# Kernel optimization log

Measured on AMD Instinct MI355X. Metric: run time of the kernel, lower is better.

Reference implementation:

```python
import jax, jax.numpy as jnp
import numpy as np

N, L, FEAT = 16, 4096, 512
DIN = 21 * 14 * 3 + FEAT  # 1394
EPS = 1e-6


def setup_inputs() -> dict:
    key = jax.random.key(0)
    ks = jax.random.split(key, 12)

    def lin_w(k, i, o):
        return (jax.random.normal(k, (i, o), jnp.float32) / np.sqrt(i)).astype(jnp.float32)

    return {
        "aa": jax.random.randint(ks[0], (N, L), 0, 21),
        "pos14": jax.random.normal(ks[1], (N, L, 14, 3), jnp.float32),
        "atom_mask": jax.random.bernoulli(ks[2], 0.9, (N, L, 14)),
        "embed": (jax.random.normal(ks[3], (21, FEAT), jnp.float32) * 0.02),
        "w1": lin_w(ks[4], DIN, 2 * FEAT),
        "b1": jnp.zeros((2 * FEAT,), jnp.float32),
        "w2": lin_w(ks[5], 2 * FEAT, FEAT),
        "b2": jnp.zeros((FEAT,), jnp.float32),
        "w3": lin_w(ks[6], FEAT, FEAT),
        "b3": jnp.zeros((FEAT,), jnp.float32),
        "w4": lin_w(ks[7], FEAT, FEAT),
        "b4": jnp.zeros((FEAT,), jnp.float32),
    }


def _normalize(v):
    return v / (jnp.linalg.norm(v, axis=-1, keepdims=True) + EPS)


def reference(aa, pos14, atom_mask, embed, w1, b1, w2, b2, w3, b3, w4, b4):
    n, l = aa.shape
    # --- frame construction: center=CA (atom 1), p1=C (atom 2), p2=N (atom 0)
    center = pos14[:, :, 1]
    v1 = pos14[:, :, 2] - center
    e1 = _normalize(v1)
    v2 = pos14[:, :, 0] - center
    u2 = v2 - jnp.sum(e1 * v2, axis=-1, keepdims=True) * e1  # Gram-Schmidt
    e2 = _normalize(u2)
    e3 = jnp.cross(e1, e2)
    R = jnp.stack([e1, e2, e3], axis=-1)  # (N,L,3,3), columns [e1,e2,e3]

    # --- global_to_local: p = R^T (q - t)
    q = pos14 - center[:, :, None, :]            # (N,L,14,3)
    crd14 = jnp.einsum('nlij,nlai->nlaj', R, q)  # (N,L,14,3)
    crd14 = jnp.where(atom_mask[..., None], crd14, 0.0)

    # --- one-hot residue placement (equivalent to the (N,L,21,14,3) expand+where)
    onehot = jax.nn.one_hot(aa, 21, dtype=crd14.dtype)             # (N,L,21)
    crd_feat = (onehot[..., None] * crd14.reshape(n, l, 1, 14 * 3))
    crd_feat = crd_feat.reshape(n, l, 21 * 14 * 3)                  # (N,L,882)

    aa_feat = embed[aa]                                             # (N,L,FEAT)
    h = jnp.concatenate([crd_feat, aa_feat], axis=-1)               # (N,L,1394)
    h = jax.nn.relu(h @ w1 + b1)
    h = jax.nn.relu(h @ w2 + b2)
    h = jax.nn.relu(h @ w3 + b3)
    return h @ w4 + b4
```

## Files before the change

### kernel.cpp

```cpp
#include <hip/hip_runtime.h>
#include <hip/hip_bf16.h>


typedef __attribute__((ext_vector_type(8))) short short8;
typedef __attribute__((ext_vector_type(4))) float floatx4;

#define TOKENS 65536
#define FEATD 512
#define L1OUT 1024
#define NAA 21
#define EPSF 1e-6f
#define ORDER_N 66880

static __device__ __forceinline__ unsigned short f2bf(float f) {
  union { float f; unsigned int u; } v; v.f = f;
  unsigned int u = v.u;
  return (unsigned short)((u + 0x7FFFu + ((u >> 16) & 1u)) >> 16);
}

#define GLDS16(g, l) __builtin_amdgcn_global_load_lds(                        \
    (const __attribute__((address_space(1))) unsigned int*)(g),               \
    (__attribute__((address_space(3))) unsigned int*)(l), 16, 0, 0)

__global__ void k_init(int* __restrict__ order, int* __restrict__ counts,
                       const unsigned int* __restrict__ mask) {
  int i = blockIdx.x * 256 + threadIdx.x;
  if (i < ORDER_N) order[i] = -1;
  if (blockIdx.x == 0) {
    if (threadIdx.x < 64) counts[threadIdx.x] = 0;
    __syncthreads();
    unsigned int v = mask[threadIdx.x];
    int b = 0;
    if (v == 0x3F800000u) b = 2;
    else if (v > 1u) b = 1;
    if (b) atomicOr(&counts[32], b);
  }
}

__global__ void k_prep(const float* __restrict__ w2, unsigned short* __restrict__ w2T,
                       const float* __restrict__ w3, unsigned short* __restrict__ w3T,
                       const float* __restrict__ w4, unsigned short* __restrict__ w4T,
                       const float* __restrict__ w1, unsigned short* __restrict__ w1T2,
                       const float* __restrict__ embed, const float* __restrict__ b1,
                       float* __restrict__ T1) {
  const int b = blockIdx.x;
  const int tid = threadIdx.x;
  if (b < 4096) {
    const float* W; unsigned short* WT; int kbits, N, idx;
    if (b < 2048)      { W = w2; WT = w2T; kbits = 10; N = 512; idx = b * 256 + tid; }
    else if (b < 3072) { W = w3; WT = w3T; kbits = 9;  N = 512; idx = (b - 2048) * 256 + tid; }
    else               { W = w4; WT = w4T; kbits = 9;  N = 512; idx = (b - 3072) * 256 + tid; }
    int K = 1 << kbits;
    int n = idx >> kbits, k = idx & (K - 1);
    WT[(size_t)n * K + k] = f2bf(W[(size_t)k * N + n]);
  } else if (b < 4180) {
    int idx = (b - 4096) * 256 + tid;
    int a = idx >> 10, c = idx & 1023;
    unsigned short tmp[64];
#pragma unroll
    for (int k = 0; k < 64; ++k)
      tmp[k] = (k < 42) ? f2bf(w1[(size_t)(a * 42 + k) * L1OUT + c]) : 0;
    uint4* dst = (uint4*)&w1T2[(size_t)idx * 64];
#pragma unroll
    for (int q = 0; q < 8; ++q) dst[q] = ((const uint4*)tmp)[q];
  } else {
    int idx = (b - 4180) * 256 + tid;
    int a = idx >> 10, c = idx & 1023;
    float acc = b1[c];
    const float* e = embed + a * FEATD;
#pragma unroll 8
    for (int k = 0; k < FEATD; ++k)
      acc += e[k] * w1[(size_t)(882 + k) * L1OUT + c];
    T1[idx] = acc;
  }
}

__global__ void k_feat(const float* __restrict__ pos14, const int* __restrict__ aa,
                       const void* __restrict__ maskp, unsigned short* __restrict__ crdb,
                       int* __restrict__ counts) {
  __shared__ int hist[NAA];
  const int tid = threadIdx.x;
  if (tid < NAA) hist[tid] = 0;
  __syncthreads();
  const int t = blockIdx.x * 256 + tid;
  const int fl = counts[32];
  const float* p = pos14 + (size_t)t * 42;
  float px[14], py[14], pz[14];
#pragma unroll
  for (int a = 0; a < 14; ++a) { px[a] = p[a*3]; py[a] = p[a*3+1]; pz[a] = p[a*3+2]; }
  float cx = px[1], cy = py[1], cz = pz[1];
  float v1x = px[2]-cx, v1y = py[2]-cy, v1z = pz[2]-cz;
  float n1 = sqrtf(v1x*v1x + v1y*v1y + v1z*v1z);
  float i1 = 1.f / (n1 + EPSF);
  float e1x = v1x*i1, e1y = v1y*i1, e1z = v1z*i1;
  float v2x = px[0]-cx, v2y = py[0]-cy, v2z = pz[0]-cz;
  float d12 = e1x*v2x + e1y*v2y + e1z*v2z;
  float u2x = v2x - d12*e1x, u2y = v2y - d12*e1y, u2z = v2z - d12*e1z;
  float n2 = sqrtf(u2x*u2x + u2y*u2y + u2z*u2z);
  float i2 = 1.f / (n2 + EPSF);
  float e2x = u2x*i2, e2y = u2y*i2, e2z = u2z*i2;
  float e3x = e1y*e2z - e1z*e2y;
  float e3y = e1z*e2x - e1x*e2z;
  float e3z = e1x*e2y - e1y*e2x;
  unsigned short ob[64];
#pragma unroll
  for (int a = 0; a < 14; ++a) {
    bool mv;
    size_t mi = (size_t)t * 14 + a;
    if (fl & 2)      mv = ((const float*)maskp)[mi] != 0.f;
    else if (fl & 1) mv = ((const unsigned char*)maskp)[mi] != 0;
    else             mv = ((const int*)maskp)[mi] != 0;
    float qx = px[a]-cx, qy = py[a]-cy, qz = pz[a]-cz;
    ob[a*3+0] = mv ? f2bf(e1x*qx + e1y*qy + e1z*qz) : 0;
    ob[a*3+1] = mv ? f2bf(e2x*qx + e2y*qy + e2z*qz) : 0;
    ob[a*3+2] = mv ? f2bf(e3x*qx + e3y*qy + e3z*qz) : 0;
  }
#pragma unroll
  for (int k = 42; k < 64; ++k) ob[k] = 0;
  uint4* dst = (uint4*)&crdb[(size_t)t * 64];
#pragma unroll
  for (int q = 0; q < 8; ++q) dst[q] = ((const uint4*)ob)[q];
  atomicAdd(&hist[aa[t]], 1);
  __syncthreads();
  if (tid < NAA && hist[tid]) atomicAdd(&counts[tid], hist[tid]);
}

__global__ void k_offsets(const int* __restrict__ counts, int* __restrict__ cnt2) {
  if (threadIdx.x == 0) {
    int run = 0;
    for (int a = 0; a < NAA; ++a) { cnt2[a] = run; run += ((counts[a] + 63) >> 6) << 6; }
  }
}

__global__ void k_scatter(const int* __restrict__ aa, int* __restrict__ cnt2,
                          int* __restrict__ order) {
  __shared__ int lh[NAA], base[NAA];
  const int tid = threadIdx.x;
  if (tid < NAA) lh[tid] = 0;
  __syncthreads();
  const int t = blockIdx.x * 256 + tid;
  const int a = aa[t];
  const int r = atomicAdd(&lh[a], 1);
  __syncthreads();
  if (tid < NAA) base[tid] = lh[tid] ? atomicAdd(&cnt2[tid], lh[tid]) : 0;
  __syncthreads();
  order[base[a] + r] = t;
}

__global__ void k_layer1(const int* __restrict__ order, const int* __restrict__ aa_g,
                         const unsigned short* __restrict__ crdb,
                         const unsigned short* __restrict__ w1T2,
                         const float* __restrict__ T1, unsigned short* __restrict__ h1) {
  __shared__ int tokens[64];
  __shared__ int s_aa;
  __shared__ unsigned short Al[64 * 64];
  __shared__ unsigned short Bl[256 * 64];
  const int tid = threadIdx.x;
  const int lane = tid & 63;
  const int wid = tid >> 6;
  const int pb = blockIdx.y;
  const int cc = blockIdx.x * 256;
  if (tid < 64) tokens[tid] = order[pb * 64 + tid];
  __syncthreads();
  if (tid == 0) {
    int a = -1;
    for (int i = 0; i < 64; ++i) if (tokens[i] >= 0) { a = aa_g[tokens[i]]; break; }
    s_aa = a;
  }
  __syncthreads();
  const int a = s_aa;
  if (a < 0) return;
  const int lrow = lane >> 3;
  const int gch = (lane & 7) ^ lrow;
#pragma unroll
  for (int i = 0; i < 2; ++i) {
    int row = wid * 16 + i * 8;
    int tok = tokens[row + lrow]; if (tok < 0) tok = 0;
    GLDS16(&crdb[(size_t)tok * 64 + gch * 8], &Al[row * 64]);
  }
  const unsigned short* bsrc = w1T2 + ((size_t)a * L1OUT + cc) * 64;
#pragma unroll
  for (int i = 0; i < 8; ++i) {
    int row = wid * 64 + i * 8;
    GLDS16(&bsrc[(size_t)(row + lrow) * 64 + gch * 8], &Bl[row * 64]);
  }
  __syncthreads();
  const int wn = wid * 64;
  floatx4 acc[4][4] = {};
#pragma unroll
  for (int kk = 0; kk < 2; ++kk) {
    short8 af[4], bfr[4];
    const int kc = kk * 4 + (lane >> 4);
#pragma unroll
    for (int i = 0; i < 4; ++i) {
      int ar = i * 16 + (lane & 15);
      af[i]  = *(const short8*)&Al[ar * 64 + (kc ^ (ar & 7)) * 8];
      int br = wn + i * 16 + (lane & 15);
      bfr[i] = *(const short8*)&Bl[br * 64 + (kc ^ (br & 7)) * 8];
    }
#pragma unroll
    for (int i = 0; i < 4; ++i)
#pragma unroll
      for (int j = 0; j < 4; ++j)
        acc[i][j] = __builtin_amdgcn_mfma_f32_16x16x32_bf16(af[i], bfr[j], acc[i][j], 0, 0, 0);
  }
#pragma unroll
  for (int i = 0; i < 4; ++i) {
    int tb = i * 16 + ((lane >> 4) << 2);
#pragma unroll
    for (int j = 0; j < 4; ++j) {
      int colg = cc + wn + j * 16 + (lane & 15);
      float bv = T1[a * L1OUT + colg];
#pragma unroll
      for (int r = 0; r < 4; ++r) {
        int tok = tokens[tb + r];
        if (tok < 0) continue;
        h1[(size_t)tok * L1OUT + colg] = f2bf(fmaxf(acc[i][j][r] + bv, 0.f));
      }
    }
  }
}

template<int K, bool RELU, bool OUTBF16>
__global__ void k_gemm(const unsigned short* __restrict__ A,
                       const unsigned short* __restrict__ BT,
                       const float* __restrict__ bias, void* __restrict__ outp) {
  constexpr int N = 512;
  __shared__ unsigned short Al[128 * 64];
  __shared__ unsigned short Bl[128 * 64];
  const int l = blockIdx.x;
  const int m0 = (((l >> 5) << 3) | (l & 7)) * 128;
  const int n0 = ((l >> 3) & 3) * 128;
  const int tid = threadIdx.x;
  const int lane = tid & 63;
  const int wid = tid >> 6;
  const int wm = (wid & 1) * 64;
  const int wn = (wid >> 1) * 64;
  const int srow = wid * 32;
  const int lrow = lane >> 3;
  const int gcol = ((lane & 7) ^ lrow) * 8;
  floatx4 acc[4][4] = {};
  for (int k0 = 0; k0 < K; k0 += 64) {
#pragma unroll
    for (int i = 0; i < 4; ++i) {
      const int row = srow + i * 8;
      GLDS16(&A [(size_t)(m0 + row + lrow) * K + k0 + gcol], &Al[row * 64]);
      GLDS16(&BT[(size_t)(n0 + row + lrow) * K + k0 + gcol], &Bl[row * 64]);
    }
    __syncthreads();
#pragma unroll
    for (int kk = 0; kk < 2; ++kk) {
      short8 af[4], bfr[4];
      const int kc = kk * 4 + (lane >> 4);
      const int swz = (kc ^ (lane & 7)) * 8;
#pragma unroll
      for (int i = 0; i < 4; ++i) {
        af[i]  = *(const short8*)&Al[(wm + i * 16 + (lane & 15)) * 64 + swz];
        bfr[i] = *(const short8*)&Bl[(wn + i * 16 + (lane & 15)) * 64 + swz];
      }
#pragma unroll
      for (int i = 0; i < 4; ++i)
#pragma unroll
        for (int j = 0; j < 4; ++j)
          acc[i][j] = __builtin_amdgcn_mfma_f32_16x16x32_bf16(af[i], bfr[j], acc[i][j], 0, 0, 0);
    }
    __syncthreads();
  }
#pragma unroll
  for (int i = 0; i < 4; ++i) {
    int rbase = m0 + wm + i * 16 + ((lane >> 4) << 2);
#pragma unroll
    for (int j = 0; j < 4; ++j) {
      int col = n0 + wn + j * 16 + (lane & 15);
      float bv = bias[col];
#pragma unroll
      for (int r = 0; r < 4; ++r) {
        float v = acc[i][j][r] + bv;
        if (RELU) v = fmaxf(v, 0.f);
        size_t off = (size_t)(rbase + r) * N + col;
        if (OUTBF16) ((unsigned short*)outp)[off] = f2bf(v);
        else ((float*)outp)[off] = v;
      }
    }
  }
}

extern "C" void kernel_launch(void* const* d_in, const int* in_sizes, int n_in,
                              void* d_out, int out_size, void* d_ws, size_t ws_size,
                              hipStream_t stream) {
  const int*   aa    = (const int*)d_in[0];
  const float* pos14 = (const float*)d_in[1];
  const void*  mask  = d_in[2];
  const float* embed = (const float*)d_in[3];
  const float* w1    = (const float*)d_in[4];
  const float* b1    = (const float*)d_in[5];
  const float* w2    = (const float*)d_in[6];
  const float* b2    = (const float*)d_in[7];
  const float* w3    = (const float*)d_in[8];
  const float* b3    = (const float*)d_in[9];
  const float* w4    = (const float*)d_in[10];
  const float* b4    = (const float*)d_in[11];

  char* ws = (char*)d_ws;
  size_t o = 0;
  auto alloc = [&](size_t b) { size_t r = o; o += (b + 255) & ~(size_t)255; return r; };
  unsigned short* w2T = (unsigned short*)(ws + alloc((size_t)512 * 1024 * 2));
  unsigned short* w3T = (unsigned short*)(ws + alloc((size_t)512 * 512 * 2));
  unsigned short* w4T = (unsigned short*)(ws + alloc((size_t)512 * 512 * 2));
  unsigned short* w1T2 = (unsigned short*)(ws + alloc((size_t)NAA * 1024 * 64 * 2));
  float* T1   = (float*)(ws + alloc((size_t)NAA * 1024 * 4));
  unsigned short* crdb = (unsigned short*)(ws + alloc((size_t)TOKENS * 64 * 2));
  int* counts = (int*)(ws + alloc(64 * 4));
  int* cnt2   = (int*)(ws + alloc(64 * 4));
  int* order  = (int*)(ws + alloc((size_t)ORDER_N * 4));
  unsigned short* h1 = (unsigned short*)(ws + alloc((size_t)TOKENS * 1024 * 2));
  unsigned short* h2 = (unsigned short*)(ws + alloc((size_t)TOKENS * 512 * 2));
  unsigned short* h3 = h1;

  k_init<<<262, 256, 0, stream>>>(order, counts, (const unsigned int*)mask);
  k_prep<<<4264, 256, 0, stream>>>(w2, w2T, w3, w3T, w4, w4T, w1, w1T2, embed, b1, T1);
  k_feat<<<256, 256, 0, stream>>>(pos14, aa, mask, crdb, counts);
  k_offsets<<<1, 64, 0, stream>>>(counts, cnt2);
  k_scatter<<<256, 256, 0, stream>>>(aa, cnt2, order);
  k_layer1<<<dim3(4, 1045), 256, 0, stream>>>(order, aa, crdb, w1T2, T1, h1);
  k_gemm<1024, true,  true ><<<2048, 256, 0, stream>>>(h1, w2T, b2, h2);
  k_gemm<512,  true,  true ><<<2048, 256, 0, stream>>>(h2, w3T, b3, h3);
  k_gemm<512,  false, false><<<2048, 256, 0, stream>>>(h3, w4T, b4, d_out);
}
```

Measured before the change: 437.6 us.

## Rewrite dense GEMMs as 256x256 double-buffered, interleaved-prefetch MFMA kernel

Replaces the 128x128 single-buffered GEMM used for layers 2-4 with a 256x256 tile kernel of 512 threads. It uses two LDS buffers, prefetches tile t+2 during compute through staged global_load_lds calls, and waits on vmcnt instead of a full sync. The MFMA blocks are interleaved with fragment loads and raised in priority. This aims to hide global-load latency and raise data reuse per tile, at the cost of far more LDS (128KB per block) and registers, which lowers occupancy.

```diff
diff --git a/kernel.cpp b/kernel.cpp
--- a/kernel.cpp
+++ b/kernel.cpp
@@ -222,57 +222,119 @@
 }
 
 template<int K, bool RELU, bool OUTBF16>
-__global__ void k_gemm(const unsigned short* __restrict__ A,
-                       const unsigned short* __restrict__ BT,
-                       const float* __restrict__ bias, void* __restrict__ outp) {
+__global__ __launch_bounds__(512, 2)
+void k_gemm256(const unsigned short* __restrict__ A,
+               const unsigned short* __restrict__ BT,
+               const float* __restrict__ bias, void* __restrict__ outp) {
   constexpr int N = 512;
-  __shared__ unsigned short Al[128 * 64];
-  __shared__ unsigned short Bl[128 * 64];
+  constexpr int NKT = K / 64;
+  __shared__ unsigned short Al[2][256 * 64];
+  __shared__ unsigned short Bl[2][256 * 64];
   const int l = blockIdx.x;
-  const int m0 = (((l >> 5) << 3) | (l & 7)) * 128;
-  const int n0 = ((l >> 3) & 3) * 128;
+  const int x = l & 7;
+  const int c = l >> 3;
+  const int m0 = (x * 32 + (c >> 1)) * 256;
+  const int n0 = (c & 1) * 256;
   const int tid = threadIdx.x;
   const int lane = tid & 63;
   const int wid = tid >> 6;
-  const int wm = (wid & 1) * 64;
-  const int wn = (wid >> 1) * 64;
-  const int srow = wid * 32;
+  const int wm2 = (wid & 1) * 128;
+  const int wn2 = (wid >> 1) * 64;
   const int lrow = lane >> 3;
   const int gcol = ((lane & 7) ^ lrow) * 8;
-  floatx4 acc[4][4] = {};
-  for (int k0 = 0; k0 < K; k0 += 64) {
-#pragma unroll
-    for (int i = 0; i < 4; ++i) {
-      const int row = srow + i * 8;
-      GLDS16(&A [(size_t)(m0 + row + lrow) * K + k0 + gcol], &Al[row * 64]);
-      GLDS16(&BT[(size_t)(n0 + row + lrow) * K + k0 + gcol], &Bl[row * 64]);
-    }
-    __syncthreads();
-#pragma unroll
-    for (int kk = 0; kk < 2; ++kk) {
-      short8 af[4], bfr[4];
-      const int kc = kk * 4 + (lane >> 4);
-      const int swz = (kc ^ (lane & 7)) * 8;
-#pragma unroll
-      for (int i = 0; i < 4; ++i) {
-        af[i]  = *(const short8*)&Al[(wm + i * 16 + (lane & 15)) * 64 + swz];
-        bfr[i] = *(const short8*)&Bl[(wn + i * 16 + (lane & 15)) * 64 + swz];
-      }
-#pragma unroll
-      for (int i = 0; i < 4; ++i)
-#pragma unroll
-        for (int j = 0; j < 4; ++j)
-          acc[i][j] = __builtin_amdgcn_mfma_f32_16x16x32_bf16(af[i], bfr[j], acc[i][j], 0, 0, 0);
-    }
-    __syncthreads();
-  }
-#pragma unroll
-  for (int i = 0; i < 4; ++i) {
-    int rbase = m0 + wm + i * 16 + ((lane >> 4) << 2);
+  const int ln = lane & 15;
+  const int sw0 = (((lane >> 4)    ) ^ (lane & 7)) * 8;
+  const int sw1 = ((4 + (lane >> 4)) ^ (lane & 7)) * 8;
+
+  const unsigned short* Ab = A  + (size_t)m0 * K;
+  const unsigned short* Bb = BT + (size_t)n0 * K;
+
+#define STAGE_A(kt, b, i)                                                     \
+  { const int row_ = (i) * 64 + wid * 8;                                      \
+    GLDS16(&Ab[(size_t)(row_ + lrow) * K + (kt) * 64 + gcol],                 \
+           &Al[b][row_ * 64]); }
+#define STAGE_B(kt, b, i)                                                     \
+  { const int row_ = (i) * 64 + wid * 8;                                      \
+    GLDS16(&Bb[(size_t)(row_ + lrow) * K + (kt) * 64 + gcol],                 \
+           &Bl[b][row_ * 64]); }
+
+  floatx4 acc[8][4] = {};
+
+#pragma unroll
+  for (int i = 0; i < 4; ++i) STAGE_A(0, 0, i);
+#pragma unroll
+  for (int i = 0; i < 4; ++i) STAGE_B(0, 0, i);
+#pragma unroll
+  for (int i = 0; i < 4; ++i) STAGE_A(1, 1, i);
+#pragma unroll
+  for (int i = 0; i < 4; ++i) STAGE_B(1, 1, i);
+
+  for (int t = 0; t < NKT; ++t) {
+    const int cur = t & 1;
+    if (t + 1 < NKT) { asm volatile("s_waitcnt vmcnt(8)" ::: "memory"); }
+    else             { asm volatile("s_waitcnt vmcnt(0)" ::: "memory"); }
+    __builtin_amdgcn_s_barrier();
+    __builtin_amdgcn_sched_barrier(0);
+    const unsigned short* Ac = &Al[cur][0];
+    const unsigned short* Bc = &Bl[cur][0];
+    const bool pf = (t + 2 < NKT);
+    short8 af[4][2], bq[2][2];
+
+#define LDA(frbase)                                                           \
+    _Pragma("unroll")                                                         \
+    for (int f = 0; f < 4; ++f) {                                             \
+      const int ro = (wm2 + ((frbase) + f) * 16 + ln) * 64;                   \
+      af[f][0] = *(const short8*)&Ac[ro + sw0];                               \
+      af[f][1] = *(const short8*)&Ac[ro + sw1];                               \
+    }
+#define LDB(fcbase)                                                           \
+    _Pragma("unroll")                                                         \
+    for (int cj = 0; cj < 2; ++cj) {                                          \
+      const int ro = (wn2 + ((fcbase) + cj) * 16 + ln) * 64;                  \
+      bq[cj][0] = *(const short8*)&Bc[ro + sw0];                              \
+      bq[cj][1] = *(const short8*)&Bc[ro + sw1];                              \
+    }
+#define MM(frbase, fcbase)                                                    \
+    __builtin_amdgcn_s_barrier();                                             \
+    __builtin_amdgcn_s_setprio(1);                                            \
+    _Pragma("unroll")                                                         \
+    for (int f = 0; f < 4; ++f)                                               \
+      _Pragma("unroll")                                                       \
+      for (int cj = 0; cj < 2; ++cj) {                                        \
+        acc[(frbase) + f][(fcbase) + cj] =                                    \
+          __builtin_amdgcn_mfma_f32_16x16x32_bf16(                            \
+            af[f][0], bq[cj][0], acc[(frbase) + f][(fcbase) + cj], 0, 0, 0);  \
+        acc[(frbase) + f][(fcbase) + cj] =                                    \
+          __builtin_amdgcn_mfma_f32_16x16x32_bf16(                            \
+            af[f][1], bq[cj][1], acc[(frbase) + f][(fcbase) + cj], 0, 0, 0);  \
+      }                                                                       \
+    __builtin_amdgcn_s_setprio(0);                                            \
+    __builtin_amdgcn_s_barrier();
+
+    LDA(0); LDB(0); MM(0, 0);
+    if (pf) { STAGE_A(t + 2, cur, 0); STAGE_A(t + 2, cur, 2); }
+    LDB(2); MM(0, 2);
+    LDA(4); MM(4, 2);
+    if (pf) { STAGE_A(t + 2, cur, 1); STAGE_A(t + 2, cur, 3); }
+    LDB(0); MM(4, 0);
+    if (pf) {
+      STAGE_B(t + 2, cur, 0); STAGE_B(t + 2, cur, 1);
+      STAGE_B(t + 2, cur, 2); STAGE_B(t + 2, cur, 3);
+    }
+#undef LDA
+#undef LDB
+#undef MM
+  }
+#undef STAGE_A
+#undef STAGE_B
+
+#pragma unroll
+  for (int i = 0; i < 8; ++i) {
+    const int rbase = m0 + wm2 + i * 16 + ((lane >> 4) << 2);
 #pragma unroll
     for (int j = 0; j < 4; ++j) {
-      int col = n0 + wn + j * 16 + (lane & 15);
-      float bv = bias[col];
+      const int col = n0 + wn2 + j * 16 + ln;
+      const float bv = bias[col];
 #pragma unroll
       for (int r = 0; r < 4; ++r) {
         float v = acc[i][j][r] + bv;
@@ -323,7 +385,7 @@
   k_offsets<<<1, 64, 0, stream>>>(counts, cnt2);
   k_scatter<<<256, 256, 0, stream>>>(aa, cnt2, order);
   k_layer1<<<dim3(4, 1045), 256, 0, stream>>>(order, aa, crdb, w1T2, T1, h1);
-  k_gemm<1024, true,  true ><<<2048, 256, 0, stream>>>(h1, w2T, b2, h2);
-  k_gemm<512,  true,  true ><<<2048, 256, 0, stream>>>(h2, w3T, b3, h3);
-  k_gemm<512,  false, false><<<2048, 256, 0, stream>>>(h3, w4T, b4, d_out);
-}
+  k_gemm256<1024, true,  true ><<<512, 512, 0, stream>>>(h1, w2T, b2, h2);
+  k_gemm256<512,  true,  true ><<<512, 512, 0, stream>>>(h2, w3T, b3, h3);
+  k_gemm256<512,  false, false><<<512, 512, 0, stream>>>(h3, w4T, b4, d_out);
+}
```

New measurement: 435.5 us. Within noise of the previous version (-0.5%).

## Use 256x256-tile double-buffered MFMA GEMM for layers two and three

Applied to the files above, without the earlier changes.

Adds a new GEMM kernel with 256x256 output tiles, 512 threads, double-buffered LDS staged through global_load_lds, XOR-swizzled LDS reads, and an interleaved prefetch/MFMA schedule with priority hints. Layers two and three switch to it, while the last fp32-output layer keeps the old kernel. Larger tiles raise operand reuse per byte loaded, and the explicit schedule tries to hide load latency behind MFMA work. In exchange, LDS use is large (128KB per block), occupancy drops to one block per CU, and only 512 blocks are launched.

```diff
diff --git a/kernel.cpp b/kernel.cpp
--- a/kernel.cpp
+++ b/kernel.cpp
@@ -285,6 +285,147 @@
   }
 }
 
+template<int K, bool RELU, bool OUTBF16>
+__global__ __launch_bounds__(512)
+void k_gemm256(const unsigned short* __restrict__ A,
+               const unsigned short* __restrict__ BT,
+               const float* __restrict__ bias, void* __restrict__ outp) {
+  constexpr int N = 512;
+  constexpr int NKT = K / 64;
+  constexpr int NITER = NKT / 2;
+  __shared__ unsigned short Al[2][256 * 64];
+  __shared__ unsigned short Bl[2][256 * 64];
+  const int l = blockIdx.x;
+  const int x = l & 7;
+  const int c = l >> 3;
+  const int m0 = (x * 32 + (c >> 1)) * 256;
+  const int n0 = (c & 1) * 256;
+  const int tid = threadIdx.x;
+  const int lane = tid & 63;
+  const int wid = tid >> 6;
+  const int wm2 = (wid & 1) * 128;
+  const int wn2 = (wid >> 1) * 64;
+  const int lrow = lane >> 3;
+  const int gcol = ((lane & 7) ^ lrow) * 8;
+  const int ln = lane & 15;
+  const int sw0 = (((lane >> 4)    ) ^ (lane & 7)) * 8;
+  const int sw1 = ((4 + (lane >> 4)) ^ (lane & 7)) * 8;
+
+  const unsigned short* Ab = A  + (size_t)m0 * K;
+  const unsigned short* Bb = BT + (size_t)n0 * K;
+
+#define STAGE_A(B, kt, i)                                                     \
+  { const int row_ = (i) * 64 + wid * 8;                                      \
+    GLDS16(&Ab[(size_t)(row_ + lrow) * K + (size_t)(kt) * 64 + gcol],         \
+           &Al[B][row_ * 64]); }
+#define STAGE_B(B, kt, i)                                                     \
+  { const int row_ = (i) * 64 + wid * 8;                                      \
+    GLDS16(&Bb[(size_t)(row_ + lrow) * K + (size_t)(kt) * 64 + gcol],         \
+           &Bl[B][row_ * 64]); }
+#define LDA(B, frbase, dst)                                                   \
+  _Pragma("unroll")                                                           \
+  for (int f = 0; f < 4; ++f) {                                               \
+    const int ro = (wm2 + ((frbase) + f) * 16 + ln) * 64;                     \
+    dst[f][0] = *(const short8*)&Al[B][ro + sw0];                             \
+    dst[f][1] = *(const short8*)&Al[B][ro + sw1];                             \
+  }
+#define LDB(B, fcbase, dst)                                                   \
+  _Pragma("unroll")                                                           \
+  for (int cj = 0; cj < 2; ++cj) {                                            \
+    const int ro = (wn2 + ((fcbase) + cj) * 16 + ln) * 64;                    \
+    dst[cj][0] = *(const short8*)&Bl[B][ro + sw0];                            \
+    dst[cj][1] = *(const short8*)&Bl[B][ro + sw1];                            \
+  }
+#define MMQ(frbase, fcbase, af, bq)                                           \
+  __builtin_amdgcn_s_setprio(1);                                              \
+  _Pragma("unroll")                                                           \
+  for (int kk = 0; kk < 2; ++kk)                                              \
+    _Pragma("unroll")                                                         \
+    for (int f = 0; f < 4; ++f)                                               \
+      _Pragma("unroll")                                                       \
+      for (int cj = 0; cj < 2; ++cj)                                          \
+        acc[(frbase) + f][(fcbase) + cj] =                                    \
+          __builtin_amdgcn_mfma_f32_16x16x32_bf16(                            \
+            af[f][kk], bq[cj][kk], acc[(frbase) + f][(fcbase) + cj], 0, 0, 0);\
+  __builtin_amdgcn_s_setprio(0);
+
+#define TILE4(B, kt2, dopf, WNend)                                            \
+  LDA(B, 0, afA); LDB(B, 0, bqA);                                             \
+  __builtin_amdgcn_sched_barrier(0);                                          \
+  __builtin_amdgcn_s_barrier();                                               \
+  MMQ(0, 0, afA, bqA);                                                        \
+  __builtin_amdgcn_s_barrier();                                               \
+  __builtin_amdgcn_sched_barrier(0);                                          \
+  if (dopf) { STAGE_A(B, kt2, 0); STAGE_A(B, kt2, 2); }                       \
+  LDA(B, 4, afB);                                                             \
+  __builtin_amdgcn_sched_barrier(0);                                          \
+  __builtin_amdgcn_s_barrier();                                               \
+  MMQ(4, 0, afB, bqA);                                                        \
+  __builtin_amdgcn_s_barrier();                                               \
+  __builtin_amdgcn_sched_barrier(0);                                          \
+  if (dopf) { STAGE_A(B, kt2, 1); STAGE_A(B, kt2, 3); }                       \
+  LDB(B, 2, bqB);                                                             \
+  __builtin_amdgcn_sched_barrier(0);                                          \
+  __builtin_amdgcn_s_barrier();                                               \
+  MMQ(4, 2, afB, bqB);                                                        \
+  __builtin_amdgcn_s_barrier();                                               \
+  __builtin_amdgcn_sched_barrier(0);                                          \
+  if (dopf) { STAGE_B(B, kt2, 0); STAGE_B(B, kt2, 1);                         \
+              STAGE_B(B, kt2, 2); STAGE_B(B, kt2, 3); }                       \
+  MMQ(0, 2, afA, bqB);                                                        \
+  asm volatile("s_waitcnt vmcnt(" #WNend ")" ::: "memory");                   \
+  __builtin_amdgcn_s_barrier();
+
+  floatx4 acc[8][4] = {};
+  short8 afA[4][2], afB[4][2], bqA[2][2], bqB[2][2];
+
+#pragma unroll
+  for (int i = 0; i < 4; ++i) STAGE_A(0, 0, i);
+#pragma unroll
+  for (int i = 0; i < 4; ++i) STAGE_B(0, 0, i);
+#pragma unroll
+  for (int i = 0; i < 4; ++i) STAGE_A(1, 1, i);
+#pragma unroll
+  for (int i = 0; i < 4; ++i) STAGE_B(1, 1, i);
+  asm volatile("s_waitcnt vmcnt(8)" ::: "memory");
+  __builtin_amdgcn_s_barrier();
+
+  for (int it = 0; it < NITER; ++it) {
+    const int te = 2 * it;
+    if (it + 1 < NITER) {
+      TILE4(0, te + 2, true, 8)
+      TILE4(1, te + 3, true, 8)
+    } else {
+      TILE4(0, te + 2, false, 0)
+      TILE4(1, te + 3, false, 0)
+    }
+  }
+#undef TILE4
+#undef MMQ
+#undef LDA
+#undef LDB
+#undef STAGE_A
+#undef STAGE_B
+
+#pragma unroll
+  for (int i = 0; i < 8; ++i) {
+    const int rbase = m0 + wm2 + i * 16 + ((lane >> 4) << 2);
+#pragma unroll
+    for (int j = 0; j < 4; ++j) {
+      const int col = n0 + wn2 + j * 16 + ln;
+      const float bv = bias[col];
+#pragma unroll
+      for (int r = 0; r < 4; ++r) {
+        float v = acc[i][j][r] + bv;
+        if (RELU) v = fmaxf(v, 0.f);
+        size_t off = (size_t)(rbase + r) * N + col;
+        if (OUTBF16) ((unsigned short*)outp)[off] = f2bf(v);
+        else ((float*)outp)[off] = v;
+      }
+    }
+  }
+}
+
 extern "C" void kernel_launch(void* const* d_in, const int* in_sizes, int n_in,
                               void* d_out, int out_size, void* d_ws, size_t ws_size,
                               hipStream_t stream) {
@@ -323,7 +464,7 @@
   k_offsets<<<1, 64, 0, stream>>>(counts, cnt2);
   k_scatter<<<256, 256, 0, stream>>>(aa, cnt2, order);
   k_layer1<<<dim3(4, 1045), 256, 0, stream>>>(order, aa, crdb, w1T2, T1, h1);
-  k_gemm<1024, true,  true ><<<2048, 256, 0, stream>>>(h1, w2T, b2, h2);
-  k_gemm<512,  true,  true ><<<2048, 256, 0, stream>>>(h2, w3T, b3, h3);
-  k_gemm<512,  false, false><<<2048, 256, 0, stream>>>(h3, w4T, b4, d_out);
-}
+  k_gemm256<1024, true,  true ><<<512, 512, 0, stream>>>(h1, w2T, b2, h2);
+  k_gemm256<512,  true,  true ><<<512, 512, 0, stream>>>(h2, w3T, b3, h3);
+  k_gemm<512, false, false><<<2048, 256, 0, stream>>>(h3, w4T, b4, d_out);
+}
```

Result: slower. 990.2 us (+126.2%).

## Fuse per-residue layer-1 GEMM into layer-2 GEMM, eliminating h1 buffer

Applied to the files above, without the earlier changes.

Replaces the separate layer-1 kernel and the first dense GEMM with one kernel that computes each 64-column chunk of h1 in shared memory from coordinate features and per-residue-type weights, then feeds it straight into the layer-2 MFMA accumulation. This removes writing and re-reading the large bf16 h1 intermediate from global memory. In exchange, layer-1 work is recomputed by each of the four output-column blocks, and a software-pipelined loop adds synchronization and LDS pressure. The order buffer is padded to match the 128-token tiling.

```diff
diff --git a/kernel.cpp b/kernel.cpp
--- a/kernel.cpp
+++ b/kernel.cpp
@@ -10,7 +10,7 @@
 #define L1OUT 1024
 #define NAA 21
 #define EPSF 1e-6f
-#define ORDER_N 66880
+#define ORDER_N 67072
 
 static __device__ __forceinline__ unsigned short f2bf(float f) {
   union { float f; unsigned int u; } v; v.f = f;
@@ -25,7 +25,7 @@
 __global__ void k_init(int* __restrict__ order, int* __restrict__ counts,
                        const unsigned int* __restrict__ mask) {
   int i = blockIdx.x * 256 + threadIdx.x;
-  if (i < ORDER_N) order[i] = -1;
+  order[i] = -1;
   if (blockIdx.x == 0) {
     if (threadIdx.x < 64) counts[threadIdx.x] = 0;
     __syncthreads();
@@ -147,80 +147,6 @@
   order[base[a] + r] = t;
 }
 
-__global__ void k_layer1(const int* __restrict__ order, const int* __restrict__ aa_g,
-                         const unsigned short* __restrict__ crdb,
-                         const unsigned short* __restrict__ w1T2,
-                         const float* __restrict__ T1, unsigned short* __restrict__ h1) {
-  __shared__ int tokens[64];
-  __shared__ int s_aa;
-  __shared__ unsigned short Al[64 * 64];
-  __shared__ unsigned short Bl[256 * 64];
-  const int tid = threadIdx.x;
-  const int lane = tid & 63;
-  const int wid = tid >> 6;
-  const int pb = blockIdx.y;
-  const int cc = blockIdx.x * 256;
-  if (tid < 64) tokens[tid] = order[pb * 64 + tid];
-  __syncthreads();
-  if (tid == 0) {
-    int a = -1;
-    for (int i = 0; i < 64; ++i) if (tokens[i] >= 0) { a = aa_g[tokens[i]]; break; }
-    s_aa = a;
-  }
-  __syncthreads();
-  const int a = s_aa;
-  if (a < 0) return;
-  const int lrow = lane >> 3;
-  const int gch = (lane & 7) ^ lrow;
-#pragma unroll
-  for (int i = 0; i < 2; ++i) {
-    int row = wid * 16 + i * 8;
-    int tok = tokens[row + lrow]; if (tok < 0) tok = 0;
-    GLDS16(&crdb[(size_t)tok * 64 + gch * 8], &Al[row * 64]);
-  }
-  const unsigned short* bsrc = w1T2 + ((size_t)a * L1OUT + cc) * 64;
-#pragma unroll
-  for (int i = 0; i < 8; ++i) {
-    int row = wid * 64 + i * 8;
-    GLDS16(&bsrc[(size_t)(row + lrow) * 64 + gch * 8], &Bl[row * 64]);
-  }
-  __syncthreads();
-  const int wn = wid * 64;
-  floatx4 acc[4][4] = {};
-#pragma unroll
-  for (int kk = 0; kk < 2; ++kk) {
-    short8 af[4], bfr[4];
-    const int kc = kk * 4 + (lane >> 4);
-#pragma unroll
-    for (int i = 0; i < 4; ++i) {
-      int ar = i * 16 + (lane & 15);
-      af[i]  = *(const short8*)&Al[ar * 64 + (kc ^ (ar & 7)) * 8];
-      int br = wn + i * 16 + (lane & 15);
-      bfr[i] = *(const short8*)&Bl[br * 64 + (kc ^ (br & 7)) * 8];
-    }
-#pragma unroll
-    for (int i = 0; i < 4; ++i)
-#pragma unroll
-      for (int j = 0; j < 4; ++j)
-        acc[i][j] = __builtin_amdgcn_mfma_f32_16x16x32_bf16(af[i], bfr[j], acc[i][j], 0, 0, 0);
-  }
-#pragma unroll
-  for (int i = 0; i < 4; ++i) {
-    int tb = i * 16 + ((lane >> 4) << 2);
-#pragma unroll
-    for (int j = 0; j < 4; ++j) {
-      int colg = cc + wn + j * 16 + (lane & 15);
-      float bv = T1[a * L1OUT + colg];
-#pragma unroll
-      for (int r = 0; r < 4; ++r) {
-        int tok = tokens[tb + r];
-        if (tok < 0) continue;
-        h1[(size_t)tok * L1OUT + colg] = f2bf(fmaxf(acc[i][j][r] + bv, 0.f));
-      }
-    }
-  }
-}
-
 template<int K, bool RELU, bool OUTBF16>
 __global__ void k_gemm(const unsigned short* __restrict__ A,
                        const unsigned short* __restrict__ BT,
@@ -285,6 +211,183 @@
   }
 }
 
+__global__ __launch_bounds__(256, 2)
+void k_gemm1f(const int* __restrict__ order, const int* __restrict__ aa_g,
+              const unsigned short* __restrict__ crdb,
+              const unsigned short* __restrict__ w1T2,
+              const float* __restrict__ T1,
+              const unsigned short* __restrict__ w2T,
+              const float* __restrict__ b2,
+              unsigned short* __restrict__ h2) {
+  constexpr int K = 1024, N = 512, NC = 16;
+  __shared__ int tokens[128];
+  __shared__ int s_aa[2];
+  __shared__ unsigned short crd[128 * 64];
+  __shared__ unsigned short W1s[2 * 64 * 64];
+  __shared__ unsigned short Ah[128 * 64];
+  __shared__ unsigned short Bl[128 * 64];
+  const int tid  = threadIdx.x;
+  const int lane = tid & 63;
+  const int wid  = tid >> 6;
+  const int m0g  = (blockIdx.x >> 2) * 128;
+  const int n0   = (blockIdx.x & 3) * 128;
+  const int lrow = lane >> 3;
+  const int gcol = ((lane & 7) ^ lrow) * 8;
+  const int ln   = lane & 15;
+  const int l4   = lane >> 4;
+
+  if (tid < 128) tokens[tid] = order[m0g + tid];
+  __syncthreads();
+  if (tid < 2) {
+    int a = -1;
+#pragma unroll 1
+    for (int i = 0; i < 64; ++i) {
+      int t = tokens[tid * 64 + i];
+      if (t >= 0) { a = aa_g[t]; break; }
+    }
+    s_aa[tid] = a < 0 ? 0 : a;
+  }
+  __syncthreads();
+  const int a0 = s_aa[0], a1 = s_aa[1];
+  const int pa = (wid < 2) ? a0 : a1;
+
+#pragma unroll
+  for (int q = 0; q < 4; ++q) {
+    const int u = q * 4 + wid;
+    const int rb = u * 8;
+    int tok = tokens[rb + lrow]; if (tok < 0) tok = 0;
+    GLDS16(&crdb[(size_t)tok * 64 + gcol], &crd[rb * 64]);
+  }
+#define STAGE_S(kc)                                                           \
+  _Pragma("unroll")                                                           \
+  for (int q = 0; q < 4; ++q) {                                               \
+    const int u = q * 4 + wid;                                                \
+    const int sl = u >> 3, sr = (u & 7) * 8;                                  \
+    const int aev = sl ? a1 : a0;                                             \
+    GLDS16(&w1T2[(size_t)(aev * 1024 + (kc) * 64 + sr + lrow) * 64 + gcol],   \
+           &W1s[(sl * 64 + sr) * 64]);                                        \
+  }
+#define STAGE_B(kc)                                                           \
+  _Pragma("unroll")                                                           \
+  for (int q = 0; q < 4; ++q) {                                               \
+    const int rb = (q * 4 + wid) * 8;                                         \
+    GLDS16(&w2T[(size_t)(n0 + rb + lrow) * K + (kc) * 64 + gcol],             \
+           &Bl[rb * 64]);                                                     \
+  }
+  STAGE_S(0)
+  asm volatile("s_waitcnt vmcnt(0)" ::: "memory");
+  __builtin_amdgcn_sched_barrier(0);
+  __syncthreads();
+
+#define PRODUCE(kc)                                                           \
+  {                                                                           \
+    floatx4 pacc[4][2] = {};                                                  \
+    short8 pb[2][2];                                                          \
+    _Pragma("unroll")                                                         \
+    for (int jj = 0; jj < 2; ++jj) {                                          \
+      const int ro = ((2 * wid + jj) * 16 + ln) * 64;                         \
+      pb[jj][0] = *(const short8*)&crd[ro + ((l4    ) ^ (lane & 7)) * 8];     \
+      pb[jj][1] = *(const short8*)&crd[ro + ((4 + l4) ^ (lane & 7)) * 8];     \
+    }                                                                         \
+    _Pragma("unroll")                                                         \
+    for (int kk = 0; kk < 2; ++kk)                                            \
+      _Pragma("unroll")                                                       \
+      for (int i = 0; i < 4; ++i) {                                           \
+        const int ro = ((pa == a1 && wid >= 2 ? 64 : 0) + i * 16 + ln) * 64;  \
+        const short8 pav = *(const short8*)&W1s[((wid < 2 ? 0 : 64) + i * 16  \
+            + ln) * 64 + (((kk * 4 + l4)) ^ (lane & 7)) * 8];                 \
+        (void)ro;                                                             \
+        _Pragma("unroll")                                                     \
+        for (int jj = 0; jj < 2; ++jj)                                        \
+          pacc[i][jj] = __builtin_amdgcn_mfma_f32_16x16x32_bf16(              \
+              pav, pb[jj][kk], pacc[i][jj], 0, 0, 0);                         \
+      }                                                                       \
+    _Pragma("unroll")                                                         \
+    for (int i = 0; i < 4; ++i) {                                             \
+      const float4 tb = *(const float4*)&T1[pa * 1024 + (kc) * 64 + i * 16    \
+                                            + (l4 << 2)];                     \
+      _Pragma("unroll")                                                       \
+      for (int jj = 0; jj < 2; ++jj) {                                        \
+        const int token = (2 * wid + jj) * 16 + ln;                           \
+        const int s = i * 16 + (l4 << 2);                                     \
+        const int phys = (((s >> 3) ^ (token & 7)) << 3) + (s & 7);           \
+        unsigned int u0 = (unsigned int)f2bf(fmaxf(pacc[i][jj][0] + tb.x, 0.f))\
+                        | ((unsigned int)f2bf(fmaxf(pacc[i][jj][1] + tb.y, 0.f)) << 16); \
+        unsigned int u1 = (unsigned int)f2bf(fmaxf(pacc[i][jj][2] + tb.z, 0.f))\
+                        | ((unsigned int)f2bf(fmaxf(pacc[i][jj][3] + tb.w, 0.f)) << 16); \
+        uint2* wp = (uint2*)&Ah[token * 64 + phys];                           \
+        *wp = make_uint2(u0, u1);                                             \
+      }                                                                       \
+    }                                                                         \
+  }
+
+  PRODUCE(0)
+  STAGE_B(0)
+  STAGE_S(1)
+
+  floatx4 acc[4][4] = {};
+  const int wm = (wid & 1) * 64;
+  const int wn = (wid >> 1) * 64;
+
+#define MAIN_CHUNK                                                            \
+  {                                                                           \
+    _Pragma("unroll")                                                         \
+    for (int kk = 0; kk < 2; ++kk) {                                          \
+      short8 af[4], bfr[4];                                                   \
+      const int swz = ((kk * 4 + l4) ^ (lane & 7)) * 8;                       \
+      _Pragma("unroll")                                                       \
+      for (int i = 0; i < 4; ++i) {                                           \
+        af[i]  = *(const short8*)&Ah[(wm + i * 16 + ln) * 64 + swz];          \
+        bfr[i] = *(const short8*)&Bl[(wn + i * 16 + ln) * 64 + swz];          \
+      }                                                                       \
+      _Pragma("unroll")                                                       \
+      for (int i = 0; i < 4; ++i)                                             \
+        _Pragma("unroll")                                                     \
+        for (int j = 0; j < 4; ++j)                                           \
+          acc[i][j] = __builtin_amdgcn_mfma_f32_16x16x32_bf16(                \
+              af[i], bfr[j], acc[i][j], 0, 0, 0);                             \
+    }                                                                         \
+  }
+
+#pragma unroll 1
+  for (int kc = 0; kc < NC - 1; ++kc) {
+    asm volatile("s_waitcnt vmcnt(4)" ::: "memory");
+    __builtin_amdgcn_sched_barrier(0);
+    __syncthreads();
+    MAIN_CHUNK
+    __syncthreads();
+    asm volatile("s_waitcnt vmcnt(0)" ::: "memory");
+    __builtin_amdgcn_sched_barrier(0);
+    PRODUCE(kc + 1)
+    STAGE_B(kc + 1)
+    if (kc + 2 < NC) STAGE_S(kc + 2)
+  }
+  asm volatile("s_waitcnt vmcnt(0)" ::: "memory");
+  __builtin_amdgcn_sched_barrier(0);
+  __syncthreads();
+  MAIN_CHUNK
+#undef MAIN_CHUNK
+#undef PRODUCE
+#undef STAGE_S
+#undef STAGE_B
+
+#pragma unroll
+  for (int i = 0; i < 4; ++i) {
+    const int trow = wm + i * 16 + (l4 << 2);
+#pragma unroll
+    for (int j = 0; j < 4; ++j) {
+      const int col = n0 + wn + j * 16 + ln;
+      const float bv = b2[col];
+#pragma unroll
+      for (int r = 0; r < 4; ++r) {
+        const int tok = tokens[trow + r];
+        if (tok < 0) continue;
+        h2[(size_t)tok * N + col] = f2bf(fmaxf(acc[i][j][r] + bv, 0.f));
+      }
+    }
+  }
+}
+
 extern "C" void kernel_launch(void* const* d_in, const int* in_sizes, int n_in,
                               void* d_out, int out_size, void* d_ws, size_t ws_size,
                               hipStream_t stream) {
@@ -313,17 +416,15 @@
   int* counts = (int*)(ws + alloc(64 * 4));
   int* cnt2   = (int*)(ws + alloc(64 * 4));
   int* order  = (int*)(ws + alloc((size_t)ORDER_N * 4));
-  unsigned short* h1 = (unsigned short*)(ws + alloc((size_t)TOKENS * 1024 * 2));
   unsigned short* h2 = (unsigned short*)(ws + alloc((size_t)TOKENS * 512 * 2));
-  unsigned short* h3 = h1;
+  unsigned short* h3 = (unsigned short*)(ws + alloc((size_t)TOKENS * 512 * 2));
 
   k_init<<<262, 256, 0, stream>>>(order, counts, (const unsigned int*)mask);
   k_prep<<<4264, 256, 0, stream>>>(w2, w2T, w3, w3T, w4, w4T, w1, w1T2, embed, b1, T1);
   k_feat<<<256, 256, 0, stream>>>(pos14, aa, mask, crdb, counts);
   k_offsets<<<1, 64, 0, stream>>>(counts, cnt2);
   k_scatter<<<256, 256, 0, stream>>>(aa, cnt2, order);
-  k_layer1<<<dim3(4, 1045), 256, 0, stream>>>(order, aa, crdb, w1T2, T1, h1);
-  k_gemm<1024, true,  true ><<<2048, 256, 0, stream>>>(h1, w2T, b2, h2);
-  k_gemm<512,  true,  true ><<<2048, 256, 0, stream>>>(h2, w3T, b3, h3);
-  k_gemm<512,  false, false><<<2048, 256, 0, stream>>>(h3, w4T, b4, d_out);
-}
+  k_gemm1f<<<(ORDER_N / 128) * 4, 256, 0, stream>>>(order, aa, crdb, w1T2, T1, w2T, b2, h2);
+  k_gemm<512, true,  true ><<<2048, 256, 0, stream>>>(h2, w3T, b3, h3);
+  k_gemm<512, false, false><<<2048, 256, 0, stream>>>(h3, w4T, b4, d_out);
+}
```

Measured after the change: 519.8 us. 1.19x slower.
